# Optimization experiments

Measured on AMD Instinct MI355X. Metric: run time of the kernel, lower is better.

## Reference

```python
import jax, jax.numpy as jnp
import numpy as np

B, I, O, N = 65536, 256, 32, 8


def chebyshev_basis(x, n):
    """Chebyshev polynomials T_0..T_{n-1} of x. x: [B, I] -> [B, I, n]."""
    T = [jnp.ones_like(x), x]
    for _ in range(n - 2):
        T.append(2.0 * x * T[-1] - T[-2])
    return jnp.stack(T[:n], axis=-1)


def setup_inputs() -> dict:
    key = jax.random.key(0)
    k1, k2 = jax.random.split(key)
    # inputs live on [-1, 1], the natural Chebyshev domain
    x = jax.random.uniform(k1, (B, I), jnp.float32, minval=-1.0, maxval=1.0)
    # weight init mirrors torch: uniform(-weight_magnitude/in, weight_magnitude/in)
    w = jax.random.uniform(k2, (O, I, N), jnp.float32, minval=-1.0 / I, maxval=1.0 / I)
    return {"x": x, "w": w}


def reference(x, w):
    n = w.shape[-1]
    phi = chebyshev_basis(x, n)          # [B, I, n] basis expansion
    out = jnp.einsum("bin,oin->bo", phi, w)  # weighted contraction
    return out
```

## Files before the change

kernel.cpp:

```cpp
#include <hip/hip_runtime.h>
#include <hip/hip_bf16.h>


typedef __attribute__((ext_vector_type(8)))  short bf16x8;
typedef __attribute__((ext_vector_type(16))) float f32x16;
typedef __attribute__((ext_vector_type(4)))  float f32x4;

__device__ __forceinline__ short f2b(float f) {
    __hip_bfloat16 h = __float2bfloat16(f);
    short s;
    __builtin_memcpy(&s, &h, sizeof(s));
    return s;
}

__global__ __launch_bounds__(256) void prep_w_kernel(const float* __restrict__ w,
                                                     short* __restrict__ wB) {
    int idx = blockIdx.x * 256 + threadIdx.x;
    int kc2 = idx >> 9;
    int l   = (idx >> 3) & 63;
    int jj  = idx & 7;
    int o = l & 31, g = l >> 5;
    int i = 2 * kc2 + (jj >> 2);
    int n = 4 * g + (jj & 3);
    wB[idx] = f2b(w[(o * 256 + i) * 8 + n]);
}

__global__ __launch_bounds__(256) void cheb_mm_kernel(const float* __restrict__ x,
                                                      const short* __restrict__ wB,
                                                      float* __restrict__ out) {
    __shared__ float smem[16384];
    const int tid = threadIdx.x;
    const int wv  = tid >> 6;
    const int l   = tid & 63;
    const int g   = l >> 5;
    const int r0  = l & 31;
    const long long row0 = (long long)blockIdx.x * 64;

    {
        const float2* xg = (const float2*)x + row0 * 128;
        float2* s2 = (float2*)smem;
        #pragma unroll
        for (int it = 0; it < 32; ++it) {
            int f = it * 256 + tid;
            int r = f >> 7, p = f & 127;
            float2 v = xg[f];
            s2[r * 128 + (p ^ (r & 15))] = v;
        }
    }
    __syncthreads();

    f32x16 acc0{};
    f32x16 acc1{};
    const float2* s2 = (const float2*)smem;
    const bf16x8* wBv = (const bf16x8*)wB;

    #pragma unroll 4
    for (int t = 0; t < 32; ++t) {
        const int kc2 = wv * 32 + t;
        const bf16x8 bfrag = wBv[kc2 * 64 + l];
        #pragma unroll
        for (int rt = 0; rt < 2; ++rt) {
            const int row = rt * 32 + r0;
            const float2 xv = s2[row * 128 + (kc2 ^ (row & 15))];
            const float xa = xv.x, xb = xv.y;
            const float x2a = xa + xa, x2b = xb + xb;
            const float a2 = x2a * xa - 1.f;
            const float a3 = x2a * a2 - xa;
            const float a4 = x2a * a3 - a2;
            const float a5 = x2a * a4 - a3;
            const float b2 = x2b * xb - 1.f;
            const float b3 = x2b * b2 - xb;
            const float b4 = x2b * b3 - b2;
            const float b5 = x2b * b4 - b3;
            const float ua0 = g ? a4 : 1.f;
            const float ua1 = g ? a5 : xa;
            const float ua2 = x2a * ua1 - ua0;
            const float ua3 = x2a * ua2 - ua1;
            const float ub0 = g ? b4 : 1.f;
            const float ub1 = g ? b5 : xb;
            const float ub2 = x2b * ub1 - ub0;
            const float ub3 = x2b * ub2 - ub1;
            bf16x8 afrag;
            afrag[0] = f2b(ua0); afrag[1] = f2b(ua1);
            afrag[2] = f2b(ua2); afrag[3] = f2b(ua3);
            afrag[4] = f2b(ub0); afrag[5] = f2b(ub1);
            afrag[6] = f2b(ub2); afrag[7] = f2b(ub3);
            if (rt == 0)
                acc0 = __builtin_amdgcn_mfma_f32_32x32x16_bf16(afrag, bfrag, acc0, 0, 0, 0);
            else
                acc1 = __builtin_amdgcn_mfma_f32_32x32x16_bf16(afrag, bfrag, acc1, 0, 0, 0);
        }
    }

    __syncthreads();
    #pragma unroll
    for (int rt = 0; rt < 2; ++rt) {
        const f32x16 a = rt ? acc1 : acc0;
        #pragma unroll
        for (int r = 0; r < 16; ++r) {
            const int rloc = (r & 3) + 8 * (r >> 2) + 4 * g;
            smem[wv * 2048 + (rt * 32 + rloc) * 32 + r0] = a[r];
        }
    }
    __syncthreads();

    {
        float* op = out + row0 * 32;
        #pragma unroll
        for (int h = 0; h < 2; ++h) {
            const int f = tid * 8 + h * 4;
            f32x4 v0 = *(const f32x4*)&smem[f];
            f32x4 v1 = *(const f32x4*)&smem[2048 + f];
            f32x4 v2 = *(const f32x4*)&smem[4096 + f];
            f32x4 v3 = *(const f32x4*)&smem[6144 + f];
            f32x4 s = (v0 + v1) + (v2 + v3);
            *(f32x4*)(op + f) = s;
        }
    }
}

extern "C" void kernel_launch(void* const* d_in, const int* in_sizes, int n_in,
                              void* d_out, int out_size, void* d_ws, size_t ws_size,
                              hipStream_t stream) {
    const float* x = (const float*)d_in[0];
    const float* w = (const float*)d_in[1];
    float* out = (float*)d_out;
    short* wB = (short*)d_ws;

    prep_w_kernel<<<256, 256, 0, stream>>>(w, wB);
    cheb_mm_kernel<<<1024, 256, 0, stream>>>(x, wB, out);
}
```

Baseline: 32.10 us.

## Split K across chunks per block with register-staged prefetch, drop cross-wave reduction

Each block now handles 128 rows, with each wave owning 32 rows over the full K dimension instead of splitting K across waves. This removes the shared-memory cross-wave reduction. x is streamed in four K-chunks through a half-size LDS buffer, and the next chunk is prefetched into registers while the current one is computed. This trades the reduction and LDS footprint for more barriers per block, half as many blocks, and uncoalesced scalar output stores.

```diff
diff --git a/kernel.cpp b/kernel.cpp
--- a/kernel.cpp
+++ b/kernel.cpp
@@ -4,7 +4,6 @@
 
 typedef __attribute__((ext_vector_type(8)))  short bf16x8;
 typedef __attribute__((ext_vector_type(16))) float f32x16;
-typedef __attribute__((ext_vector_type(4)))  float f32x4;
 
 __device__ __forceinline__ short f2b(float f) {
     __hip_bfloat16 h = __float2bfloat16(f);
@@ -28,40 +27,52 @@
 __global__ __launch_bounds__(256) void cheb_mm_kernel(const float* __restrict__ x,
                                                       const short* __restrict__ wB,
                                                       float* __restrict__ out) {
-    __shared__ float smem[16384];
+    __shared__ float smem[8192];
     const int tid = threadIdx.x;
     const int wv  = tid >> 6;
     const int l   = tid & 63;
     const int g   = l >> 5;
     const int r0  = l & 31;
-    const long long row0 = (long long)blockIdx.x * 64;
+    const long long rowB = (long long)blockIdx.x * 128;
 
-    {
-        const float2* xg = (const float2*)x + row0 * 128;
-        float2* s2 = (float2*)smem;
+    const float4* xg4 = (const float4*)x;
+    float2* s2 = (float2*)smem;
+
+    float4 stg[8];
+
+    auto LOAD = [&](int c) {
         #pragma unroll
-        for (int it = 0; it < 32; ++it) {
-            int f = it * 256 + tid;
-            int r = f >> 7, p = f & 127;
-            float2 v = xg[f];
-            s2[r * 128 + (p ^ (r & 15))] = v;
+        for (int q = 0; q < 8; ++q) {
+            int S = q * 256 + tid;
+            int row = S >> 4, f4 = S & 15;
+            stg[q] = xg4[(rowB + row) * 64 + c * 16 + f4];
         }
-    }
-    __syncthreads();
+    };
+    auto WRITE = [&]() {
+        #pragma unroll
+        for (int q = 0; q < 8; ++q) {
+            int S = q * 256 + tid;
+            int row = S >> 4, f4 = S & 15;
+            int p0 = (2 * f4)     ^ (row & 31);
+            int p1 = (2 * f4 + 1) ^ (row & 31);
+            s2[row * 32 + p0] = make_float2(stg[q].x, stg[q].y);
+            s2[row * 32 + p1] = make_float2(stg[q].z, stg[q].w);
+        }
+    };
 
-    f32x16 acc0{};
-    f32x16 acc1{};
-    const float2* s2 = (const float2*)smem;
+    LOAD(0); WRITE(); __syncthreads();
+
+    f32x16 acc{};
     const bf16x8* wBv = (const bf16x8*)wB;
+    const float2* srow = s2 + (wv * 32 + r0) * 32;
 
-    #pragma unroll 4
-    for (int t = 0; t < 32; ++t) {
-        const int kc2 = wv * 32 + t;
-        const bf16x8 bfrag = wBv[kc2 * 64 + l];
-        #pragma unroll
-        for (int rt = 0; rt < 2; ++rt) {
-            const int row = rt * 32 + r0;
-            const float2 xv = s2[row * 128 + (kc2 ^ (row & 15))];
+    for (int c = 0; c < 4; ++c) {
+        if (c < 3) LOAD(c + 1);
+        #pragma unroll 8
+        for (int t = 0; t < 32; ++t) {
+            const int kc2 = c * 32 + t;
+            const bf16x8 bfrag = wBv[kc2 * 64 + l];
+            const float2 xv = srow[t ^ r0];
             const float xa = xv.x, xb = xv.y;
             const float x2a = xa + xa, x2b = xb + xb;
             const float a2 = x2a * xa - 1.f;
@@ -85,37 +96,17 @@
             afrag[2] = f2b(ua2); afrag[3] = f2b(ua3);
             afrag[4] = f2b(ub0); afrag[5] = f2b(ub1);
             afrag[6] = f2b(ub2); afrag[7] = f2b(ub3);
-            if (rt == 0)
-                acc0 = __builtin_amdgcn_mfma_f32_32x32x16_bf16(afrag, bfrag, acc0, 0, 0, 0);
-            else
-                acc1 = __builtin_amdgcn_mfma_f32_32x32x16_bf16(afrag, bfrag, acc1, 0, 0, 0);
+            acc = __builtin_amdgcn_mfma_f32_32x32x16_bf16(afrag, bfrag, acc, 0, 0, 0);
         }
+        __syncthreads();
+        if (c < 3) { WRITE(); __syncthreads(); }
     }
 
-    __syncthreads();
+    float* op = out + (rowB + wv * 32) * 32 + r0;
     #pragma unroll
-    for (int rt = 0; rt < 2; ++rt) {
-        const f32x16 a = rt ? acc1 : acc0;
-        #pragma unroll
-        for (int r = 0; r < 16; ++r) {
-            const int rloc = (r & 3) + 8 * (r >> 2) + 4 * g;
-            smem[wv * 2048 + (rt * 32 + rloc) * 32 + r0] = a[r];
-        }
-    }
-    __syncthreads();
-
-    {
-        float* op = out + row0 * 32;
-        #pragma unroll
-        for (int h = 0; h < 2; ++h) {
-            const int f = tid * 8 + h * 4;
-            f32x4 v0 = *(const f32x4*)&smem[f];
-            f32x4 v1 = *(const f32x4*)&smem[2048 + f];
-            f32x4 v2 = *(const f32x4*)&smem[4096 + f];
-            f32x4 v3 = *(const f32x4*)&smem[6144 + f];
-            f32x4 s = (v0 + v1) + (v2 + v3);
-            *(f32x4*)(op + f) = s;
-        }
+    for (int r = 0; r < 16; ++r) {
+        const int rloc = (r & 3) + 8 * (r >> 2) + 4 * g;
+        op[rloc * 32] = acc[r];
     }
 }
 
@@ -128,5 +119,5 @@
     short* wB = (short*)d_ws;
 
     prep_w_kernel<<<256, 256, 0, stream>>>(w, wB);
-    cheb_mm_kernel<<<1024, 256, 0, stream>>>(x, wB, out);
+    cheb_mm_kernel<<<512, 256, 0, stream>>>(x, wB, out);
 }
```

Measured after the change: 49.01 us. 1.53x slower.
